# Optimization experiments

Hardware: AMD Instinct MI355X
Metric: run time of the kernel (lower is better)

## Reference

```python
import jax, jax.numpy as jnp
import numpy as np

H = 64  # hidden_layers

def _lstm_cell(x, h, c, Wih, Whh, bih, bhh):
    # PyTorch LSTMCell: gates ordered i, f, g, o
    gates = x @ Wih.T + bih + h @ Whh.T + bhh  # (B, 4H)
    i, f, g, o = jnp.split(gates, 4, axis=-1)
    c_new = jax.nn.sigmoid(f) * c + jax.nn.sigmoid(i) * jnp.tanh(g)
    h_new = jax.nn.sigmoid(o) * jnp.tanh(c_new)
    return h_new, c_new

def setup_inputs() -> dict:
    key = jax.random.key(0)
    ks = jax.random.split(key, 12)
    B, S = 1024, 512
    s1 = 1.0 / np.sqrt(H)
    u = lambda k, shape: jax.random.uniform(k, shape, jnp.float32, -s1, s1)
    return {
        "input_t": jax.random.normal(ks[0], (B, S), jnp.float32),
        "W_ih1": u(ks[1], (4 * H, 1)),
        "W_hh1": u(ks[2], (4 * H, H)),
        "b_ih1": u(ks[3], (4 * H,)),
        "b_hh1": u(ks[4], (4 * H,)),
        "W_ih2": u(ks[5], (4 * H, H)),
        "W_hh2": u(ks[6], (4 * H, H)),
        "b_ih2": u(ks[7], (4 * H,)),
        "b_hh2": u(ks[8], (4 * H,)),
        "W_lin": u(ks[9], (1, H)),
        "b_lin": u(ks[10], (1,)),
        "future_preds": 0,
    }

def reference(input_t, W_ih1, W_hh1, b_ih1, b_hh1, W_ih2, W_hh2, b_ih2, b_hh2,
              W_lin, b_lin, future_preds):
    B = input_t.shape[0]
    z = jnp.zeros((B, H), jnp.float32)

    def step(carry, x_t):
        h1, c1, h2, c2 = carry
        h1, c1 = _lstm_cell(x_t, h1, c1, W_ih1, W_hh1, b_ih1, b_hh1)
        h2, c2 = _lstm_cell(h1, h2, c2, W_ih2, W_hh2, b_ih2, b_hh2)
        out = h2 @ W_lin.T + b_lin  # (B, 1)
        return (h1, c1, h2, c2), out[:, 0]

    xs = input_t.T[:, :, None]  # (S, B, 1)
    carry, outs = jax.lax.scan(step, (z, z, z, z), xs)
    outputs = outs.T  # (B, S)

    if future_preds > 0:  # static Python int
        def step_ar(carry_o, _):
            (h1, c1, h2, c2), out = carry_o
            h1, c1 = _lstm_cell(out, h1, c1, W_ih1, W_hh1, b_ih1, b_hh1)
            h2, c2 = _lstm_cell(h1, h2, c2, W_ih2, W_hh2, b_ih2, b_hh2)
            out = h2 @ W_lin.T + b_lin
            return ((h1, c1, h2, c2), out), out[:, 0]

        last = outs[-1][:, None]  # (B, 1)
        _, outs2 = jax.lax.scan(step_ar, (carry, last), None, length=future_preds)
        outputs = jnp.concatenate([outputs, outs2.T], axis=1)
    return outputs
```

## Files before the change

kernel.cpp:

```cpp
#include <hip/hip_runtime.h>
#include <stdint.h>

#define HD   64
#define SEQ  512
#define BTCH 1024
#define NB   16
#define NBLK (BTCH / NB)
#define HSTR 72

typedef _Float16 f16x8 __attribute__((ext_vector_type(8)));
typedef float    f32x4 __attribute__((ext_vector_type(4)));

union FragU { uint32_t u[4]; uint4 q; f16x8 v; };

static __device__ __forceinline__ float rcpf_(float x) {
#if __has_builtin(__builtin_amdgcn_rcpf)
    return __builtin_amdgcn_rcpf(x);
#else
    return 1.0f / x;
#endif
}
static __device__ __forceinline__ float sigmoidf_(float x) {
    return rcpf_(1.0f + __expf(-x));
}
static __device__ __forceinline__ float tanhf_(float x) {
    float e = __expf(2.0f * x);
    return (e - 1.0f) * rcpf_(e + 1.0f);
}
static __device__ __forceinline__ uint32_t pack2h(float a, float b) {
    _Float16 ha = (_Float16)a, hb = (_Float16)b;
    uint16_t ua = __builtin_bit_cast(uint16_t, ha);
    uint16_t ub = __builtin_bit_cast(uint16_t, hb);
    return (uint32_t)ua | ((uint32_t)ub << 16);
}

static __device__ __forceinline__ f16x8 make_frag(const float* __restrict__ W,
                                                  int row, int kb) {
    const float* p = W + row * HD + kb;
    FragU f;
    f.u[0] = pack2h(p[0], p[1]);
    f.u[1] = pack2h(p[2], p[3]);
    f.u[2] = pack2h(p[4], p[5]);
    f.u[3] = pack2h(p[6], p[7]);
    return f.v;
}

static __device__ __forceinline__ f16x8 read_B(const uint16_t* Hb, int n, int kb) {
    FragU f;
    f.q = *(const uint4*)(Hb + n * HSTR + kb);
    return f.v;
}

__global__ __attribute__((amdgpu_flat_work_group_size(512, 512),
                          amdgpu_waves_per_eu(2, 2)))
void lstm_mfma(const float* __restrict__ input,
               const float* __restrict__ Wih1,
               const float* __restrict__ Whh1,
               const float* __restrict__ bih1, const float* __restrict__ bhh1,
               const float* __restrict__ Wih2,
               const float* __restrict__ Whh2,
               const float* __restrict__ bih2, const float* __restrict__ bhh2,
               const float* __restrict__ Wlin,
               const float* __restrict__ blin,
               float* __restrict__ out)
{
    const int tid  = threadIdx.x;
    const int lane = tid & 63;
    const int wv   = tid >> 6;
    const int ub   = wv & 3;
    const int hf   = wv >> 2;
    const int n    = lane & 15;
    const int l4   = lane >> 4;
    const int b0   = blockIdx.x * NB;
    const int u0   = ub * 16 + l4 * 4;

    __shared__ uint16_t H1[NB * HSTR];
    __shared__ uint16_t H2[NB * HSTR];
    __shared__ float    perW[8][16];

    for (int i = tid; i < NB * HSTR; i += 512) { H1[i] = 0; H2[i] = 0; }

    f16x8 A1[4][2], A2[4][2], A3[4][2];
#pragma unroll
    for (int g = 0; g < 4; ++g) {
        int row = (g * 4 + ub) * 16 + n;
#pragma unroll
        for (int h = 0; h < 2; ++h) {
            int kb = h * 32 + l4 * 8;
            A1[g][h] = make_frag(Whh1, row, kb);
            A2[g][h] = make_frag(Wih2, row, kb);
            A3[g][h] = make_frag(Whh2, row, kb);
        }
    }

    f32x4 bias1f[4], wih1f[4], bias2f[4];
#pragma unroll
    for (int g = 0; g < 4; ++g)
#pragma unroll
        for (int r = 0; r < 4; ++r) {
            int row = g * 64 + u0 + r;
            bias1f[g][r] = bih1[row] + bhh1[row];
            wih1f[g][r]  = Wih1[row];
            bias2f[g][r] = bih2[row] + bhh2[row];
        }
    const float wl0 = Wlin[u0 + hf * 2];
    const float wl1 = Wlin[u0 + hf * 2 + 1];
    const float bl  = blin[0];

    float c1[2] = {0.f, 0.f};
    float c2[2] = {0.f, 0.f};

    const float* xp = input + (size_t)(b0 + n) * SEQ;
    float xn = xp[0];

    const int klo = l4 * 8, khi = 32 + l4 * 8;
    __syncthreads();

#pragma unroll 1
    for (int t = 0; t < SEQ; ++t) {
        const float x = xn;
        xn = xp[(t + 1) & (SEQ - 1)];

        f16x8 B1l = read_B(H1, n, klo), B1h = read_B(H1, n, khi);
        f16x8 B3l = read_B(H2, n, klo), B3h = read_B(H2, n, khi);
        f32x4 acc[4];
#pragma unroll
        for (int g = 0; g < 4; ++g) {
            acc[g] = bias1f[g] + x * wih1f[g];
            acc[g] = __builtin_amdgcn_mfma_f32_16x16x32_f16(A1[g][0], B1l, acc[g], 0, 0, 0);
            acc[g] = __builtin_amdgcn_mfma_f32_16x16x32_f16(A1[g][1], B1h, acc[g], 0, 0, 0);
        }
        float h1v[2];
#pragma unroll
        for (int rr = 0; rr < 2; ++rr) {
            int r = hf * 2 + rr;
            float i_ = sigmoidf_(acc[0][r]);
            float f_ = sigmoidf_(acc[1][r]);
            float g_ = tanhf_(acc[2][r]);
            float o_ = sigmoidf_(acc[3][r]);
            c1[rr] = f_ * c1[rr] + i_ * g_;
            h1v[rr] = o_ * tanhf_(c1[rr]);
        }
        __syncthreads();

        *(uint32_t*)(&H1[n * HSTR + u0 + hf * 2]) = pack2h(h1v[0], h1v[1]);
        __syncthreads();

        f16x8 B2l = read_B(H1, n, klo), B2h = read_B(H1, n, khi);
#pragma unroll
        for (int g = 0; g < 4; ++g) {
            acc[g] = bias2f[g];
            acc[g] = __builtin_amdgcn_mfma_f32_16x16x32_f16(A2[g][0], B2l, acc[g], 0, 0, 0);
            acc[g] = __builtin_amdgcn_mfma_f32_16x16x32_f16(A2[g][1], B2h, acc[g], 0, 0, 0);
            acc[g] = __builtin_amdgcn_mfma_f32_16x16x32_f16(A3[g][0], B3l, acc[g], 0, 0, 0);
            acc[g] = __builtin_amdgcn_mfma_f32_16x16x32_f16(A3[g][1], B3h, acc[g], 0, 0, 0);
        }
        float h2v[2];
#pragma unroll
        for (int rr = 0; rr < 2; ++rr) {
            int r = hf * 2 + rr;
            float i_ = sigmoidf_(acc[0][r]);
            float f_ = sigmoidf_(acc[1][r]);
            float g_ = tanhf_(acc[2][r]);
            float o_ = sigmoidf_(acc[3][r]);
            c2[rr] = f_ * c2[rr] + i_ * g_;
            h2v[rr] = o_ * tanhf_(c2[rr]);
        }
        *(uint32_t*)(&H2[n * HSTR + u0 + hf * 2]) = pack2h(h2v[0], h2v[1]);

        float p = h2v[0] * wl0 + h2v[1] * wl1;
        p += __shfl_xor(p, 16, 64);
        p += __shfl_xor(p, 32, 64);
        if (l4 == 0) perW[wv][n] = p;
        __syncthreads();

        if (wv == 0 && lane < 16) {
            float s = perW[0][n] + perW[1][n] + perW[2][n] + perW[3][n]
                    + perW[4][n] + perW[5][n] + perW[6][n] + perW[7][n] + bl;
            out[(size_t)(b0 + n) * SEQ + t] = s;
        }
    }
}

extern "C" void kernel_launch(void* const* d_in, const int* in_sizes, int n_in,
                              void* d_out, int out_size, void* d_ws, size_t ws_size,
                              hipStream_t stream) {
    const float* input = (const float*)d_in[0];
    const float* Wih1  = (const float*)d_in[1];
    const float* Whh1  = (const float*)d_in[2];
    const float* bih1  = (const float*)d_in[3];
    const float* bhh1  = (const float*)d_in[4];
    const float* Wih2  = (const float*)d_in[5];
    const float* Whh2  = (const float*)d_in[6];
    const float* bih2  = (const float*)d_in[7];
    const float* bhh2  = (const float*)d_in[8];
    const float* Wlin  = (const float*)d_in[9];
    const float* blin  = (const float*)d_in[10];

    float* outp = (float*)d_out;

    lstm_mfma<<<dim3(NBLK), dim3(512), 0, stream>>>(
        input, Wih1, Whh1, bih1, bhh1, Wih2, Whh2, bih2, bhh2, Wlin, blin, outp);
}
```

Baseline: 809.5 us.

## Process two batch groups per block and double-buffer H1 to drop a barrier

The kernel now gives each block 32 batch rows split into two independent groups of four waves. Previously the two wave halves repeated the same MFMAs and each applied the activations to only half the rows. Now each wave applies the gate activations to all four accumulator rows, so the MFMA work is no longer duplicated. H1 is double-buffered so the new hidden state can be written before a single barrier instead of two. The layer-2 recurrent MFMA chain is split into a separate accumulator to shorten dependency chains. In exchange, the grid is halved to 32 blocks and each wave does twice the transcendental work per step, which may lengthen the latency-bound per-step critical path.

```diff
diff --git a/kernel.cpp b/kernel.cpp
--- a/kernel.cpp
+++ b/kernel.cpp
@@ -4,8 +4,9 @@
 #define HD   64
 #define SEQ  512
 #define BTCH 1024
-#define NB   16
+#define NB   32
 #define NBLK (BTCH / NB)
+#define NGRP 2
 #define HSTR 72
 
 typedef _Float16 f16x8 __attribute__((ext_vector_type(8)));
@@ -52,7 +53,7 @@
 }
 
 __global__ __attribute__((amdgpu_flat_work_group_size(512, 512),
-                          amdgpu_waves_per_eu(2, 2)))
+                          amdgpu_waves_per_eu(1, 2)))
 void lstm_mfma(const float* __restrict__ input,
                const float* __restrict__ Wih1,
                const float* __restrict__ Whh1,
@@ -67,18 +68,19 @@
     const int tid  = threadIdx.x;
     const int lane = tid & 63;
     const int wv   = tid >> 6;
+    const int grp  = wv >> 2;
     const int ub   = wv & 3;
-    const int hf   = wv >> 2;
     const int n    = lane & 15;
     const int l4   = lane >> 4;
-    const int b0   = blockIdx.x * NB;
+    const int b0   = blockIdx.x * NB + grp * 16;
     const int u0   = ub * 16 + l4 * 4;
 
-    __shared__ uint16_t H1[NB * HSTR];
-    __shared__ uint16_t H2[NB * HSTR];
+    __shared__ uint16_t H1[2][NGRP][16 * HSTR];
+    __shared__ uint16_t H2[NGRP][16 * HSTR];
     __shared__ float    perW[8][16];
 
-    for (int i = tid; i < NB * HSTR; i += 512) { H1[i] = 0; H2[i] = 0; }
+    for (int i = tid; i < 2 * NGRP * 16 * HSTR; i += 512) ((uint16_t*)H1)[i] = 0;
+    for (int i = tid; i < NGRP * 16 * HSTR; i += 512) ((uint16_t*)H2)[i] = 0;
 
     f16x8 A1[4][2], A2[4][2], A3[4][2];
 #pragma unroll
@@ -103,12 +105,12 @@
             wih1f[g][r]  = Wih1[row];
             bias2f[g][r] = bih2[row] + bhh2[row];
         }
-    const float wl0 = Wlin[u0 + hf * 2];
-    const float wl1 = Wlin[u0 + hf * 2 + 1];
+    const float wl0 = Wlin[u0], wl1 = Wlin[u0 + 1], wl2 = Wlin[u0 + 2], wl3 = Wlin[u0 + 3];
     const float bl  = blin[0];
 
-    float c1[2] = {0.f, 0.f};
-    float c2[2] = {0.f, 0.f};
+    float c1[4] = {0.f, 0.f, 0.f, 0.f};
+    float c2[4] = {0.f, 0.f, 0.f, 0.f};
+    const f32x4 zero4 = {0.f, 0.f, 0.f, 0.f};
 
     const float* xp = input + (size_t)(b0 + n) * SEQ;
     float xn = xp[0];
@@ -121,8 +123,12 @@
         const float x = xn;
         xn = xp[(t + 1) & (SEQ - 1)];
 
-        f16x8 B1l = read_B(H1, n, klo), B1h = read_B(H1, n, khi);
-        f16x8 B3l = read_B(H2, n, klo), B3h = read_B(H2, n, khi);
+        const uint16_t* H1r = H1[t & 1][grp];
+        uint16_t*       H1w = H1[(t + 1) & 1][grp];
+        uint16_t*       H2g = H2[grp];
+
+        f16x8 B1l = read_B(H1r, n, klo), B1h = read_B(H1r, n, khi);
+        f16x8 B3l = read_B(H2g, n, klo), B3h = read_B(H2g, n, khi);
         f32x4 acc[4];
 #pragma unroll
         for (int g = 0; g < 4; ++g) {
@@ -130,53 +136,53 @@
             acc[g] = __builtin_amdgcn_mfma_f32_16x16x32_f16(A1[g][0], B1l, acc[g], 0, 0, 0);
             acc[g] = __builtin_amdgcn_mfma_f32_16x16x32_f16(A1[g][1], B1h, acc[g], 0, 0, 0);
         }
-        float h1v[2];
-#pragma unroll
-        for (int rr = 0; rr < 2; ++rr) {
-            int r = hf * 2 + rr;
+        float h1v[4];
+#pragma unroll
+        for (int r = 0; r < 4; ++r) {
             float i_ = sigmoidf_(acc[0][r]);
             float f_ = sigmoidf_(acc[1][r]);
             float g_ = tanhf_(acc[2][r]);
             float o_ = sigmoidf_(acc[3][r]);
-            c1[rr] = f_ * c1[rr] + i_ * g_;
-            h1v[rr] = o_ * tanhf_(c1[rr]);
-        }
+            c1[r] = f_ * c1[r] + i_ * g_;
+            h1v[r] = o_ * tanhf_(c1[r]);
+        }
+        uint2 hw1; hw1.x = pack2h(h1v[0], h1v[1]); hw1.y = pack2h(h1v[2], h1v[3]);
+        *(uint2*)(&H1w[n * HSTR + u0]) = hw1;
         __syncthreads();
 
-        *(uint32_t*)(&H1[n * HSTR + u0 + hf * 2]) = pack2h(h1v[0], h1v[1]);
-        __syncthreads();
-
-        f16x8 B2l = read_B(H1, n, klo), B2h = read_B(H1, n, khi);
+        f16x8 B2l = read_B(H1w, n, klo), B2h = read_B(H1w, n, khi);
+        f32x4 accB[4];
 #pragma unroll
         for (int g = 0; g < 4; ++g) {
-            acc[g] = bias2f[g];
-            acc[g] = __builtin_amdgcn_mfma_f32_16x16x32_f16(A2[g][0], B2l, acc[g], 0, 0, 0);
-            acc[g] = __builtin_amdgcn_mfma_f32_16x16x32_f16(A2[g][1], B2h, acc[g], 0, 0, 0);
-            acc[g] = __builtin_amdgcn_mfma_f32_16x16x32_f16(A3[g][0], B3l, acc[g], 0, 0, 0);
-            acc[g] = __builtin_amdgcn_mfma_f32_16x16x32_f16(A3[g][1], B3h, acc[g], 0, 0, 0);
-        }
-        float h2v[2];
-#pragma unroll
-        for (int rr = 0; rr < 2; ++rr) {
-            int r = hf * 2 + rr;
+            acc[g]  = bias2f[g];
+            acc[g]  = __builtin_amdgcn_mfma_f32_16x16x32_f16(A2[g][0], B2l, acc[g], 0, 0, 0);
+            acc[g]  = __builtin_amdgcn_mfma_f32_16x16x32_f16(A2[g][1], B2h, acc[g], 0, 0, 0);
+            accB[g] = __builtin_amdgcn_mfma_f32_16x16x32_f16(A3[g][0], B3l, zero4, 0, 0, 0);
+            accB[g] = __builtin_amdgcn_mfma_f32_16x16x32_f16(A3[g][1], B3h, accB[g], 0, 0, 0);
+            acc[g] += accB[g];
+        }
+        float h2v[4];
+#pragma unroll
+        for (int r = 0; r < 4; ++r) {
             float i_ = sigmoidf_(acc[0][r]);
             float f_ = sigmoidf_(acc[1][r]);
             float g_ = tanhf_(acc[2][r]);
             float o_ = sigmoidf_(acc[3][r]);
-            c2[rr] = f_ * c2[rr] + i_ * g_;
-            h2v[rr] = o_ * tanhf_(c2[rr]);
-        }
-        *(uint32_t*)(&H2[n * HSTR + u0 + hf * 2]) = pack2h(h2v[0], h2v[1]);
-
-        float p = h2v[0] * wl0 + h2v[1] * wl1;
+            c2[r] = f_ * c2[r] + i_ * g_;
+            h2v[r] = o_ * tanhf_(c2[r]);
+        }
+        uint2 hw2; hw2.x = pack2h(h2v[0], h2v[1]); hw2.y = pack2h(h2v[2], h2v[3]);
+        *(uint2*)(&H2g[n * HSTR + u0]) = hw2;
+
+        float p = h2v[0] * wl0 + h2v[1] * wl1 + h2v[2] * wl2 + h2v[3] * wl3;
         p += __shfl_xor(p, 16, 64);
         p += __shfl_xor(p, 32, 64);
         if (l4 == 0) perW[wv][n] = p;
         __syncthreads();
 
-        if (wv == 0 && lane < 16) {
-            float s = perW[0][n] + perW[1][n] + perW[2][n] + perW[3][n]
-                    + perW[4][n] + perW[5][n] + perW[6][n] + perW[7][n] + bl;
+        if (ub == 0 && lane < 16) {
+            float s = perW[grp * 4 + 0][n] + perW[grp * 4 + 1][n]
+                    + perW[grp * 4 + 2][n] + perW[grp * 4 + 3][n] + bl;
             out[(size_t)(b0 + n) * SEQ + t] = s;
         }
     }
```

New measurement: 991.8 us. +22.5%, slower.
